# Kernel optimization log

Hardware: AMD Instinct MI355X
Metric: run time of the kernel (lower is better)

Reference implementation:

```python
import jax, jax.numpy as jnp
import numpy as np

NEG_SLOPE = 0.2   # PyG GATConv default negative_slope
LN_EPS = 1e-5
SOFTMAX_EPS = 1e-16  # PyG softmax denominator eps


def setup_inputs() -> dict:
    key = jax.random.key(0)
    ks = jax.random.split(key, 6)
    N, IN, OUT, H, E = 100000, 128, 64, 2, 1600000
    X = jax.random.normal(ks[0], (N, IN), dtype=jnp.float32)
    edge_index = jax.random.randint(ks[1], (2, E), 0, N, dtype=jnp.int64)
    W = jax.random.normal(ks[2], (H * OUT, IN), dtype=jnp.float32) * 0.05
    att_src = jax.random.normal(ks[3], (H, OUT), dtype=jnp.float32) * 0.05
    att_dst = jax.random.normal(ks[4], (H, OUT), dtype=jnp.float32) * 0.05
    bias = jnp.zeros((OUT,), dtype=jnp.float32)
    ln_gamma = jnp.ones((OUT,), dtype=jnp.float32)
    ln_beta = jnp.zeros((OUT,), dtype=jnp.float32)
    return {"X": X, "edge_index": edge_index, "W": W, "att_src": att_src,
            "att_dst": att_dst, "bias": bias, "ln_gamma": ln_gamma, "ln_beta": ln_beta}


def reference(X, edge_index, W, att_src, att_dst, bias, ln_gamma, ln_beta):
    N = X.shape[0]
    H, F = att_src.shape
    # PyG GATConv default: add self-loops
    loops = jnp.arange(N, dtype=edge_index.dtype)
    src = jnp.concatenate([edge_index[0], loops])  # [Et]
    dst = jnp.concatenate([edge_index[1], loops])  # [Et]
    # linear projection: x' = X @ W^T  -> [N, H, F]
    x = (X @ W.T).reshape(N, H, F)
    # per-node attention logits  [N, H]
    a_src = jnp.einsum('nhf,hf->nh', x, att_src)
    a_dst = jnp.einsum('nhf,hf->nh', x, att_dst)
    # per-edge logits, leaky relu  [Et, H]
    e = jax.nn.leaky_relu(a_src[src] + a_dst[dst], NEG_SLOPE)
    # segment softmax over incoming edges of each dst node
    m = jax.ops.segment_max(e, dst, num_segments=N)          # [N, H]
    ex = jnp.exp(e - m[dst])
    denom = jax.ops.segment_sum(ex, dst, num_segments=N)     # [N, H]
    alpha = ex / (denom[dst] + SOFTMAX_EPS)                  # [Et, H]
    # weighted scatter-add of source features
    msg = x[src] * alpha[:, :, None]                         # [Et, H, F]
    out = jax.ops.segment_sum(msg, dst, num_segments=N)      # [N, H, F]
    # concat=False -> mean over heads, then bias
    out = out.mean(axis=1) + bias                            # [N, F]
    # LayerNorm over features
    mu = out.mean(axis=-1, keepdims=True)
    var = ((out - mu) ** 2).mean(axis=-1, keepdims=True)
    h = (out - mu) * jax.lax.rsqrt(var + LN_EPS) * ln_gamma + ln_beta
    return h
```

## Files before the change

kernel.cpp:

```cpp
#include <hip/hip_runtime.h>
#include <hip/hip_bf16.h>

#define NEG_SLOPE 0.2f
#define LN_EPS 1e-5f
#define SM_EPS 1e-16f

typedef __attribute__((ext_vector_type(8))) short bf16x8;
typedef __attribute__((ext_vector_type(4))) float f32x4;

__device__ inline unsigned short f2bf(float f) {
    unsigned u = __float_as_uint(f);
    return (unsigned short)((u + 0x7FFFu + ((u >> 16) & 1u)) >> 16);
}
__device__ inline float bf_lo(unsigned int v) { return __uint_as_float(v << 16); }
__device__ inline float bf_hi(unsigned int v) { return __uint_as_float(v & 0xffff0000u); }

#define NBIN 512
#define SORT_CHUNK 4096

__global__ __launch_bounds__(256) void k_gemm(const float* __restrict__ X,
                                              const float* __restrict__ W,
                                              const float* __restrict__ att_src,
                                              const float* __restrict__ att_dst,
                                              unsigned int* __restrict__ xp,
                                              float2* __restrict__ aS,
                                              float2* __restrict__ aD, int N) {
    __shared__ unsigned short Ws[128 * 136];
    __shared__ unsigned short Xs[64 * 136];
    const int t = threadIdx.x;
    const int b0 = blockIdx.x * 64;
    const int lane = t & 63;
    const int w = t >> 6;
    const int c15 = lane & 15;
    const int quad = lane >> 4;

#pragma unroll
    for (int i = 0; i < 16; ++i) {
        int f = i * 256 + t;
        int nr = f >> 5;
        int q = f & 31;
        float4 v = reinterpret_cast<const float4*>(W)[nr * 32 + q];
        ushort4 b;
        b.x = f2bf(v.x); b.y = f2bf(v.y); b.z = f2bf(v.z); b.w = f2bf(v.w);
        *reinterpret_cast<ushort4*>(&Ws[nr * 136 + q * 4]) = b;
    }
#pragma unroll
    for (int i = 0; i < 8; ++i) {
        int f = i * 256 + t;
        int m = f >> 5;
        int q = f & 31;
        int gr = b0 + m;
        if (gr >= N) gr = N - 1;
        float4 v = reinterpret_cast<const float4*>(X)[(size_t)gr * 32 + q];
        ushort4 b;
        b.x = f2bf(v.x); b.y = f2bf(v.y); b.z = f2bf(v.z); b.w = f2bf(v.w);
        *reinterpret_cast<ushort4*>(&Xs[m * 136 + q * 4]) = b;
    }
    __syncthreads();

    f32x4 acc[8];
#pragma unroll
    for (int ct = 0; ct < 8; ++ct) acc[ct] = (f32x4){0.f, 0.f, 0.f, 0.f};

#pragma unroll
    for (int kc = 0; kc < 4; ++kc) {
        bf16x8 af = *reinterpret_cast<const bf16x8*>(
            &Xs[(w * 16 + c15) * 136 + kc * 32 + quad * 8]);
#pragma unroll
        for (int ct = 0; ct < 8; ++ct) {
            bf16x8 bfr = *reinterpret_cast<const bf16x8*>(
                &Ws[(ct * 16 + c15) * 136 + kc * 32 + quad * 8]);
            acc[ct] = __builtin_amdgcn_mfma_f32_16x16x32_bf16(af, bfr, acc[ct], 0, 0, 0);
        }
    }

    float attS[8], attD[8];
#pragma unroll
    for (int ct = 0; ct < 8; ++ct) {
        attS[ct] = att_src[ct * 16 + c15];
        attD[ct] = att_dst[ct * 16 + c15];
    }

#pragma unroll
    for (int r = 0; r < 4; ++r) {
        int row = b0 + w * 16 + quad * 4 + r;
        float s0 = 0.f, s1 = 0.f, d0 = 0.f, d1 = 0.f;
#pragma unroll
        for (int ct = 0; ct < 4; ++ct) {
            s0 += acc[ct][r] * attS[ct];
            d0 += acc[ct][r] * attD[ct];
            s1 += acc[ct + 4][r] * attS[ct + 4];
            d1 += acc[ct + 4][r] * attD[ct + 4];
        }
#pragma unroll
        for (int o = 1; o < 16; o <<= 1) {
            s0 += __shfl_xor(s0, o);
            s1 += __shfl_xor(s1, o);
            d0 += __shfl_xor(d0, o);
            d1 += __shfl_xor(d1, o);
        }
        if (row < N) {
#pragma unroll
            for (int ct = 0; ct < 4; ++ct) {
                unsigned int p = (unsigned int)f2bf(acc[ct][r]) |
                                 ((unsigned int)f2bf(acc[ct + 4][r]) << 16);
                xp[(size_t)row * 64 + ct * 16 + c15] = p;
            }
            if (c15 == 0) {
                aS[row] = make_float2(s0, s1);
                aD[row] = make_float2(d0, d1);
            }
        }
    }
}

__global__ __launch_bounds__(256) void k_uw(const int* __restrict__ ei,
                                            const float2* __restrict__ aS,
                                            const float2* __restrict__ aD,
                                            unsigned int* __restrict__ uW,
                                            int* __restrict__ binTotal, int E) {
    __shared__ int hist[NBIN];
    const int t = threadIdx.x;
    for (int i = t; i < NBIN; i += 256) hist[i] = 0;
    __syncthreads();
    const int base = blockIdx.x * 2048;
#pragma unroll
    for (int k = 0; k < 8; ++k) {
        int i = base + k * 256 + t;
        if (i < E) {
            int s = ei[i];
            int d = ei[E + i];
            float2 a = aS[s];
            float2 ad2 = aD[d];
            float f0 = a.x + ad2.x; f0 = fmaxf(f0, NEG_SLOPE * f0);
            float f1 = a.y + ad2.y; f1 = fmaxf(f1, NEG_SLOPE * f1);
            uW[i] = (unsigned int)f2bf(__expf(f0)) |
                    ((unsigned int)f2bf(__expf(f1)) << 16);
            atomicAdd(&hist[d >> 8], 1);
        }
    }
    __syncthreads();
    for (int i = t; i < NBIN; i += 256)
        if (hist[i]) atomicAdd(&binTotal[i], hist[i]);
}

__global__ __launch_bounds__(512) void k_binscan(const int* __restrict__ binTotal,
                                                 int* __restrict__ binStart,
                                                 int* __restrict__ binCursor, int E) {
    __shared__ int buf[NBIN];
    const int t = threadIdx.x;
    int v = binTotal[t];
    buf[t] = v;
    __syncthreads();
    for (int o = 1; o < NBIN; o <<= 1) {
        int u = (t >= o) ? buf[t - o] : 0;
        __syncthreads();
        buf[t] += u;
        __syncthreads();
    }
    int excl = buf[t] - v;
    binStart[t] = excl;
    binCursor[t] = excl;
    if (t == NBIN - 1) binStart[NBIN] = buf[t];
}

__global__ __launch_bounds__(256) void k_scatter(const int* __restrict__ ei,
                                                 const unsigned int* __restrict__ uW,
                                                 int* __restrict__ binCursor,
                                                 uint2* __restrict__ tmp, int E) {
    __shared__ int off[NBIN];
    const int t = threadIdx.x;
    const int base = blockIdx.x * SORT_CHUNK;

    int se[16], de[16];
    unsigned int ue[16];
#pragma unroll
    for (int k = 0; k < 16; ++k) {
        int i = base + k * 256 + t;
        if (i < E) {
            se[k] = ei[i];
            de[k] = ei[E + i];
            ue[k] = uW[i];
        } else {
            de[k] = -1;
        }
    }

    for (int i = t; i < NBIN; i += 256) off[i] = 0;
    __syncthreads();
#pragma unroll
    for (int k = 0; k < 16; ++k)
        if (de[k] >= 0) atomicAdd(&off[de[k] >> 8], 1);
    __syncthreads();
    for (int i = t; i < NBIN; i += 256) {
        int h = off[i];
        off[i] = h ? atomicAdd(&binCursor[i], h) : 0;
    }
    __syncthreads();
#pragma unroll
    for (int k = 0; k < 16; ++k) {
        if (de[k] >= 0) {
            int p = atomicAdd(&off[de[k] >> 8], 1);
            tmp[p] = make_uint2(((unsigned)(de[k] & 255) << 24) | (unsigned)se[k],
                                ue[k]);
        }
    }
}

__global__ __launch_bounds__(256) void k_bucket(const uint2* __restrict__ tmp,
                                                const int* __restrict__ binStart,
                                                const float2* __restrict__ aS,
                                                const float2* __restrict__ aD,
                                                uint2* __restrict__ csr,
                                                int* __restrict__ row_ptr,
                                                float2* __restrict__ metaN,
                                                int E, int N) {
    __shared__ int cnt[256];
    __shared__ int cur[256];
    __shared__ int lds[4];
    const int t = threadIdx.x;
    const int b = blockIdx.x;
    const int start = binStart[b];
    const int end = binStart[b + 1];
    const int m = end - start;

    cnt[t] = 0;
    __syncthreads();
    for (int k = t; k < m; k += 256) {
        uint2 e = tmp[start + k];
        atomicAdd(&cnt[e.x >> 24], 1);
    }
    __syncthreads();

    int v = cnt[t];
    int lane = t & 63, w = t >> 6;
    int incl = v;
#pragma unroll
    for (int o = 1; o < 64; o <<= 1) {
        int u = __shfl_up(incl, o);
        if (lane >= o) incl += u;
    }
    if (lane == 63) lds[w] = incl;
    __syncthreads();
    if (t == 0) {
        int run = 0;
        for (int i = 0; i < 4; ++i) { int tv = lds[i]; lds[i] = run; run += tv; }
    }
    __syncthreads();
    int excl = lds[w] + incl - v;
    cur[t] = start + excl;

    int d = b * 256 + t;
    if (d < N) {
        float2 a = aS[d];
        float2 ad2 = aD[d];
        float f0 = a.x + ad2.x; f0 = fmaxf(f0, NEG_SLOPE * f0);
        float f1 = a.y + ad2.y; f1 = fmaxf(f1, NEG_SLOPE * f1);
        metaN[d] = make_float2(__expf(f0), __expf(f1));
        row_ptr[d] = start + excl;
    }
    if (b == 0 && t == 0) row_ptr[N] = E;
    __syncthreads();

    for (int k = t; k < m; k += 256) {
        uint2 e = tmp[start + k];
        int p = atomicAdd(&cur[e.x >> 24], 1);
        csr[p] = make_uint2(e.x & 0x00FFFFFFu, e.y);
    }
}

__global__ __launch_bounds__(256) void k_agg(const unsigned int* __restrict__ xp,
                                             const float2* __restrict__ metaN,
                                             const int* __restrict__ row_ptr,
                                             const uint2* __restrict__ csr,
                                             const float* __restrict__ bias,
                                             const float* __restrict__ gamma,
                                             const float* __restrict__ beta,
                                             float* __restrict__ out, int N) {
    const int w = threadIdx.x >> 6, lane = threadIdx.x & 63;
    const int n = blockIdx.x * 4 + w;
    if (n >= N) return;

    float2 meta = metaN[n];
    unsigned int vself = xp[(size_t)n * 64 + lane];
    float S0 = meta.x * bf_lo(vself);
    float S1 = meta.y * bf_hi(vself);
    float D0 = meta.x, D1 = meta.y;

    const int jb = row_ptr[n], je = row_ptr[n + 1];
    int j = jb;
    for (; j + 7 < je; j += 8) {
        int ju = __builtin_amdgcn_readfirstlane(j);
        uint2 c[8];
#pragma unroll
        for (int q = 0; q < 8; ++q) c[q] = csr[ju + q];
        unsigned int v[8];
#pragma unroll
        for (int q = 0; q < 8; ++q) v[q] = xp[(size_t)c[q].x * 64 + lane];
#pragma unroll
        for (int q = 0; q < 8; ++q) {
            float u0 = bf_lo(c[q].y), u1 = bf_hi(c[q].y);
            S0 += u0 * bf_lo(v[q]);
            S1 += u1 * bf_hi(v[q]);
            D0 += u0; D1 += u1;
        }
    }
    for (; j + 3 < je; j += 4) {
        int ju = __builtin_amdgcn_readfirstlane(j);
        uint2 c[4];
#pragma unroll
        for (int q = 0; q < 4; ++q) c[q] = csr[ju + q];
        unsigned int v[4];
#pragma unroll
        for (int q = 0; q < 4; ++q) v[q] = xp[(size_t)c[q].x * 64 + lane];
#pragma unroll
        for (int q = 0; q < 4; ++q) {
            float u0 = bf_lo(c[q].y), u1 = bf_hi(c[q].y);
            S0 += u0 * bf_lo(v[q]);
            S1 += u1 * bf_hi(v[q]);
            D0 += u0; D1 += u1;
        }
    }
    for (; j < je; ++j) {
        uint2 c = csr[__builtin_amdgcn_readfirstlane(j)];
        unsigned int vv = xp[(size_t)c.x * 64 + lane];
        float u0 = bf_lo(c.y), u1 = bf_hi(c.y);
        S0 += u0 * bf_lo(vv);
        S1 += u1 * bf_hi(vv);
        D0 += u0; D1 += u1;
    }

    float inv0 = 0.5f / (D0 + SM_EPS);
    float inv1 = 0.5f / (D1 + SM_EPS);
    float o = inv0 * S0 + inv1 * S1 + bias[lane];

    float mu = o;
#pragma unroll
    for (int d = 32; d > 0; d >>= 1) mu += __shfl_xor(mu, d);
    mu *= (1.0f / 64.0f);
    float dv = o - mu;
    float var = dv * dv;
#pragma unroll
    for (int d = 32; d > 0; d >>= 1) var += __shfl_xor(var, d);
    var *= (1.0f / 64.0f);
    out[(size_t)n * 64 + lane] = dv * rsqrtf(var + LN_EPS) * gamma[lane] + beta[lane];
}

extern "C" void kernel_launch(void* const* d_in, const int* in_sizes, int n_in,
                              void* d_out, int out_size, void* d_ws, size_t ws_size,
                              hipStream_t stream) {
    const float* X        = (const float*)d_in[0];
    const int*   ei       = (const int*)d_in[1];
    const float* W        = (const float*)d_in[2];
    const float* att_src  = (const float*)d_in[3];
    const float* att_dst  = (const float*)d_in[4];
    const float* bias     = (const float*)d_in[5];
    const float* ln_gamma = (const float*)d_in[6];
    const float* ln_beta  = (const float*)d_in[7];
    float* out = (float*)d_out;

    const int N = in_sizes[0] / 128;
    const int E = in_sizes[1] / 2;
    const int NBUCK = (N + 255) / 256;

    char* ws = (char*)d_ws;
    size_t off = 0;
    auto alloc = [&](size_t bytes) {
        size_t o = off;
        off += (bytes + 255) & ~(size_t)255;
        return o;
    };
    unsigned int* xp     = (unsigned int*)(ws + alloc((size_t)N * 64 * 4));
    float2* aS           = (float2*)(ws + alloc((size_t)N * 8));
    float2* aD           = (float2*)(ws + alloc((size_t)N * 8));
    float2* metaN        = (float2*)(ws + alloc((size_t)N * 8));
    int* row_ptr         = (int*)(ws + alloc((size_t)(N + 1) * 4));
    uint2* csr           = (uint2*)(ws + alloc((size_t)E * 8));
    uint2* tmp           = (uint2*)(ws + alloc((size_t)E * 8));
    unsigned int* uW     = (unsigned int*)(ws + alloc((size_t)E * 4));
    int* binTotal        = (int*)(ws + alloc((NBIN + 1) * 4));
    int* binStart        = (int*)(ws + alloc((NBIN + 1) * 4));
    int* binCursor       = (int*)(ws + alloc(NBIN * 4));

    hipMemsetAsync(binTotal, 0, NBIN * 4, stream);

    k_gemm<<<(N + 63) / 64, 256, 0, stream>>>(X, W, att_src, att_dst, xp, aS, aD, N);
    k_uw<<<(E + 2047) / 2048, 256, 0, stream>>>(ei, aS, aD, uW, binTotal, E);
    k_binscan<<<1, 512, 0, stream>>>(binTotal, binStart, binCursor, E);
    k_scatter<<<(E + SORT_CHUNK - 1) / SORT_CHUNK, 256, 0, stream>>>(ei, uW, binCursor, tmp, E);
    k_bucket<<<NBUCK, 256, 0, stream>>>(tmp, binStart, aS, aD, csr, row_ptr,
                                        metaN, E, N);
    k_agg<<<(N + 3) / 4, 256, 0, stream>>>(xp, metaN, row_ptr, csr,
                                           bias, ln_gamma, ln_beta, out, N);
}
```

Before: 252.1 us.

## Fuse edge weighting into scatter with fixed-capacity bins and precompute denominators

```diff
diff --git a/kernel.cpp b/kernel.cpp
--- a/kernel.cpp
+++ b/kernel.cpp
@@ -15,8 +15,9 @@
 __device__ inline float bf_lo(unsigned int v) { return __uint_as_float(v << 16); }
 __device__ inline float bf_hi(unsigned int v) { return __uint_as_float(v & 0xffff0000u); }
 
-#define NBIN 512
-#define SORT_CHUNK 4096
+#define NBIN 1024
+#define BCAP 2560
+#define SCHUNK 2048
 
 __global__ __launch_bounds__(256) void k_gemm(const float* __restrict__ X,
                                               const float* __restrict__ W,
@@ -24,7 +25,8 @@
                                               const float* __restrict__ att_dst,
                                               unsigned int* __restrict__ xp,
                                               float2* __restrict__ aS,
-                                              float2* __restrict__ aD, int N) {
+                                              float2* __restrict__ aD,
+                                              int* __restrict__ binCursor, int N) {
     __shared__ unsigned short Ws[128 * 136];
     __shared__ unsigned short Xs[64 * 136];
     const int t = threadIdx.x;
@@ -33,6 +35,10 @@
     const int w = t >> 6;
     const int c15 = lane & 15;
     const int quad = lane >> 4;
+
+    if (blockIdx.x == 0) {
+        for (int i = t; i < NBIN; i += 256) binCursor[i] = i * BCAP;
+    }
 
 #pragma unroll
     for (int i = 0; i < 16; ++i) {
@@ -114,73 +120,30 @@
     }
 }
 
-__global__ __launch_bounds__(256) void k_uw(const int* __restrict__ ei,
-                                            const float2* __restrict__ aS,
-                                            const float2* __restrict__ aD,
-                                            unsigned int* __restrict__ uW,
-                                            int* __restrict__ binTotal, int E) {
-    __shared__ int hist[NBIN];
+__global__ __launch_bounds__(256) void k_scatter(const int* __restrict__ ei,
+                                                 const float2* __restrict__ aS,
+                                                 const float2* __restrict__ aD,
+                                                 int* __restrict__ binCursor,
+                                                 uint2* __restrict__ tmp, int E) {
+    __shared__ int off[NBIN];
     const int t = threadIdx.x;
-    for (int i = t; i < NBIN; i += 256) hist[i] = 0;
-    __syncthreads();
-    const int base = blockIdx.x * 2048;
+    const int base = blockIdx.x * SCHUNK;
+
+    int se[8], de[8];
+    unsigned int ue[8];
 #pragma unroll
     for (int k = 0; k < 8; ++k) {
         int i = base + k * 256 + t;
         if (i < E) {
             int s = ei[i];
             int d = ei[E + i];
+            se[k] = s; de[k] = d;
             float2 a = aS[s];
             float2 ad2 = aD[d];
             float f0 = a.x + ad2.x; f0 = fmaxf(f0, NEG_SLOPE * f0);
             float f1 = a.y + ad2.y; f1 = fmaxf(f1, NEG_SLOPE * f1);
-            uW[i] = (unsigned int)f2bf(__expf(f0)) |
+            ue[k] = (unsigned int)f2bf(__expf(f0)) |
                     ((unsigned int)f2bf(__expf(f1)) << 16);
-            atomicAdd(&hist[d >> 8], 1);
-        }
-    }
-    __syncthreads();
-    for (int i = t; i < NBIN; i += 256)
-        if (hist[i]) atomicAdd(&binTotal[i], hist[i]);
-}
-
-__global__ __launch_bounds__(512) void k_binscan(const int* __restrict__ binTotal,
-                                                 int* __restrict__ binStart,
-                                                 int* __restrict__ binCursor, int E) {
-    __shared__ int buf[NBIN];
-    const int t = threadIdx.x;
-    int v = binTotal[t];
-    buf[t] = v;
-    __syncthreads();
-    for (int o = 1; o < NBIN; o <<= 1) {
-        int u = (t >= o) ? buf[t - o] : 0;
-        __syncthreads();
-        buf[t] += u;
-        __syncthreads();
-    }
-    int excl = buf[t] - v;
-    binStart[t] = excl;
-    binCursor[t] = excl;
-    if (t == NBIN - 1) binStart[NBIN] = buf[t];
-}
-
-__global__ __launch_bounds__(256) void k_scatter(const int* __restrict__ ei,
-                                                 const unsigned int* __restrict__ uW,
-                                                 int* __restrict__ binCursor,
-                                                 uint2* __restrict__ tmp, int E) {
-    __shared__ int off[NBIN];
-    const int t = threadIdx.x;
-    const int base = blockIdx.x * SORT_CHUNK;
-
-    int se[16], de[16];
-    unsigned int ue[16];
-#pragma unroll
-    for (int k = 0; k < 16; ++k) {
-        int i = base + k * 256 + t;
-        if (i < E) {
-            se[k] = ei[i];
-            de[k] = ei[E + i];
-            ue[k] = uW[i];
         } else {
             de[k] = -1;
         }
@@ -189,8 +152,8 @@
     for (int i = t; i < NBIN; i += 256) off[i] = 0;
     __syncthreads();
 #pragma unroll
-    for (int k = 0; k < 16; ++k)
-        if (de[k] >= 0) atomicAdd(&off[de[k] >> 8], 1);
+    for (int k = 0; k < 8; ++k)
+        if (de[k] >= 0) atomicAdd(&off[de[k] >> 7], 1);
     __syncthreads();
     for (int i = t; i < NBIN; i += 256) {
         int h = off[i];
@@ -198,80 +161,90 @@
     }
     __syncthreads();
 #pragma unroll
-    for (int k = 0; k < 16; ++k) {
+    for (int k = 0; k < 8; ++k) {
         if (de[k] >= 0) {
-            int p = atomicAdd(&off[de[k] >> 8], 1);
-            tmp[p] = make_uint2(((unsigned)(de[k] & 255) << 24) | (unsigned)se[k],
+            int p = atomicAdd(&off[de[k] >> 7], 1);
+            tmp[p] = make_uint2(((unsigned)(de[k] & 127) << 24) | (unsigned)se[k],
                                 ue[k]);
         }
     }
 }
 
 __global__ __launch_bounds__(256) void k_bucket(const uint2* __restrict__ tmp,
-                                                const int* __restrict__ binStart,
+                                                const int* __restrict__ binCursor,
                                                 const float2* __restrict__ aS,
                                                 const float2* __restrict__ aD,
                                                 uint2* __restrict__ csr,
-                                                int* __restrict__ row_ptr,
-                                                float2* __restrict__ metaN,
-                                                int E, int N) {
-    __shared__ int cnt[256];
-    __shared__ int cur[256];
-    __shared__ int lds[4];
+                                                unsigned int* __restrict__ rowPtr,
+                                                float4* __restrict__ metaN, int N) {
+    __shared__ uint2 ebuf[BCAP];
+    __shared__ int cnt[128];
+    __shared__ int cur[128];
+    __shared__ float den0[128], den1[128];
+    __shared__ int lds2[2];
     const int t = threadIdx.x;
     const int b = blockIdx.x;
-    const int start = binStart[b];
-    const int end = binStart[b + 1];
-    const int m = end - start;
-
-    cnt[t] = 0;
-    __syncthreads();
+    const int start = b * BCAP;
+    int m = binCursor[b] - start;
+    if (m > BCAP) m = BCAP;
+
+    if (t < 128) { cnt[t] = 0; den0[t] = 0.f; den1[t] = 0.f; }
+    __syncthreads();
+
     for (int k = t; k < m; k += 256) {
         uint2 e = tmp[start + k];
-        atomicAdd(&cnt[e.x >> 24], 1);
-    }
-    __syncthreads();
-
-    int v = cnt[t];
-    int lane = t & 63, w = t >> 6;
-    int incl = v;
-#pragma unroll
-    for (int o = 1; o < 64; o <<= 1) {
-        int u = __shfl_up(incl, o);
-        if (lane >= o) incl += u;
-    }
-    if (lane == 63) lds[w] = incl;
-    __syncthreads();
-    if (t == 0) {
-        int run = 0;
-        for (int i = 0; i < 4; ++i) { int tv = lds[i]; lds[i] = run; run += tv; }
-    }
-    __syncthreads();
-    int excl = lds[w] + incl - v;
-    cur[t] = start + excl;
-
-    int d = b * 256 + t;
-    if (d < N) {
-        float2 a = aS[d];
-        float2 ad2 = aD[d];
-        float f0 = a.x + ad2.x; f0 = fmaxf(f0, NEG_SLOPE * f0);
-        float f1 = a.y + ad2.y; f1 = fmaxf(f1, NEG_SLOPE * f1);
-        metaN[d] = make_float2(__expf(f0), __expf(f1));
-        row_ptr[d] = start + excl;
-    }
-    if (b == 0 && t == 0) row_ptr[N] = E;
+        ebuf[k] = e;
+        int li = e.x >> 24;
+        atomicAdd(&cnt[li], 1);
+        atomicAdd(&den0[li], bf_lo(e.y));
+        atomicAdd(&den1[li], bf_hi(e.y));
+    }
+    __syncthreads();
+
+    int v = 0, incl = 0;
+    const int lane = t & 63, w = t >> 6;
+    if (t < 128) {
+        v = cnt[t];
+        incl = v;
+#pragma unroll
+        for (int o = 1; o < 64; o <<= 1) {
+            int u = __shfl_up(incl, o);
+            if (lane >= o) incl += u;
+        }
+        if (lane == 63) lds2[w] = incl;
+    }
+    __syncthreads();
+    if (t == 0) { int a = lds2[0]; lds2[0] = 0; lds2[1] = a; }
+    __syncthreads();
+    if (t < 128) {
+        int excl = lds2[w] + incl - v;
+        cur[t] = excl;
+        int d = b * 128 + t;
+        if (d < N) {
+            float2 a = aS[d];
+            float2 ad2 = aD[d];
+            float f0 = a.x + ad2.x; f0 = fmaxf(f0, NEG_SLOPE * f0);
+            float f1 = a.y + ad2.y; f1 = fmaxf(f1, NEG_SLOPE * f1);
+            float ws0 = __expf(f0), ws1 = __expf(f1);
+            float D0 = den0[t] + ws0, D1 = den1[t] + ws1;
+            metaN[d] = make_float4(ws0, ws1,
+                                   0.5f / (D0 + SM_EPS), 0.5f / (D1 + SM_EPS));
+            rowPtr[d] = (unsigned)(start + excl) | ((unsigned)v << 22);
+        }
+    }
     __syncthreads();
 
     for (int k = t; k < m; k += 256) {
-        uint2 e = tmp[start + k];
-        int p = atomicAdd(&cur[e.x >> 24], 1);
-        csr[p] = make_uint2(e.x & 0x00FFFFFFu, e.y);
+        uint2 e = ebuf[k];
+        int li = e.x >> 24;
+        int p = atomicAdd(&cur[li], 1);
+        csr[start + p] = make_uint2(e.x & 0x00FFFFFFu, e.y);
     }
 }
 
 __global__ __launch_bounds__(256) void k_agg(const unsigned int* __restrict__ xp,
-                                             const float2* __restrict__ metaN,
-                                             const int* __restrict__ row_ptr,
+                                             const float4* __restrict__ metaN,
+                                             const unsigned int* __restrict__ rowPtr,
                                              const uint2* __restrict__ csr,
                                              const float* __restrict__ bias,
                                              const float* __restrict__ gamma,
@@ -281,13 +254,14 @@
     const int n = blockIdx.x * 4 + w;
     if (n >= N) return;
 
-    float2 meta = metaN[n];
+    float4 meta = metaN[n];
     unsigned int vself = xp[(size_t)n * 64 + lane];
     float S0 = meta.x * bf_lo(vself);
     float S1 = meta.y * bf_hi(vself);
-    float D0 = meta.x, D1 = meta.y;
-
-    const int jb = row_ptr[n], je = row_ptr[n + 1];
+
+    unsigned int pr = rowPtr[n];
+    const int jb = (int)(pr & 0x3FFFFFu);
+    const int je = jb + (int)(pr >> 22);
     int j = jb;
     for (; j + 7 < je; j += 8) {
         int ju = __builtin_amdgcn_readfirstlane(j);
@@ -299,10 +273,8 @@
         for (int q = 0; q < 8; ++q) v[q] = xp[(size_t)c[q].x * 64 + lane];
 #pragma unroll
         for (int q = 0; q < 8; ++q) {
-            float u0 = bf_lo(c[q].y), u1 = bf_hi(c[q].y);
-            S0 += u0 * bf_lo(v[q]);
-            S1 += u1 * bf_hi(v[q]);
-            D0 += u0; D1 += u1;
+            S0 += bf_lo(c[q].y) * bf_lo(v[q]);
+            S1 += bf_hi(c[q].y) * bf_hi(v[q]);
         }
     }
     for (; j + 3 < je; j += 4) {
@@ -315,24 +287,18 @@
         for (int q = 0; q < 4; ++q) v[q] = xp[(size_t)c[q].x * 64 + lane];
 #pragma unroll
         for (int q = 0; q < 4; ++q) {
-            float u0 = bf_lo(c[q].y), u1 = bf_hi(c[q].y);
-            S0 += u0 * bf_lo(v[q]);
-            S1 += u1 * bf_hi(v[q]);
-            D0 += u0; D1 += u1;
+            S0 += bf_lo(c[q].y) * bf_lo(v[q]);
+            S1 += bf_hi(c[q].y) * bf_hi(v[q]);
         }
     }
     for (; j < je; ++j) {
         uint2 c = csr[__builtin_amdgcn_readfirstlane(j)];
         unsigned int vv = xp[(size_t)c.x * 64 + lane];
-        float u0 = bf_lo(c.y), u1 = bf_hi(c.y);
-        S0 += u0 * bf_lo(vv);
-        S1 += u1 * bf_hi(vv);
-        D0 += u0; D1 += u1;
-    }
-
-    float inv0 = 0.5f / (D0 + SM_EPS);
-    float inv1 = 0.5f / (D1 + SM_EPS);
-    float o = inv0 * S0 + inv1 * S1 + bias[lane];
+        S0 += bf_lo(c.y) * bf_lo(vv);
+        S1 += bf_hi(c.y) * bf_hi(vv);
+    }
+
+    float o = meta.z * S0 + meta.w * S1 + bias[lane];
 
     float mu = o;
 #pragma unroll
@@ -361,7 +327,7 @@
 
     const int N = in_sizes[0] / 128;
     const int E = in_sizes[1] / 2;
-    const int NBUCK = (N + 255) / 256;
+    const int NBUCK = (N + 127) / 128;
 
     char* ws = (char*)d_ws;
     size_t off = 0;
@@ -373,23 +339,18 @@
     unsigned int* xp     = (unsigned int*)(ws + alloc((size_t)N * 64 * 4));
     float2* aS           = (float2*)(ws + alloc((size_t)N * 8));
     float2* aD           = (float2*)(ws + alloc((size_t)N * 8));
-    float2* metaN        = (float2*)(ws + alloc((size_t)N * 8));
-    int* row_ptr         = (int*)(ws + alloc((size_t)(N + 1) * 4));
-    uint2* csr           = (uint2*)(ws + alloc((size_t)E * 8));
-    uint2* tmp           = (uint2*)(ws + alloc((size_t)E * 8));
-    unsigned int* uW     = (unsigned int*)(ws + alloc((size_t)E * 4));
-    int* binTotal        = (int*)(ws + alloc((NBIN + 1) * 4));
-    int* binStart        = (int*)(ws + alloc((NBIN + 1) * 4));
+    float4* metaN        = (float4*)(ws + alloc((size_t)N * 16));
+    unsigned int* rowPtr = (unsigned int*)(ws + alloc((size_t)N * 4));
+    uint2* csr           = (uint2*)(ws + alloc((size_t)NBIN * BCAP * 8));
+    uint2* tmp           = (uint2*)(ws + alloc((size_t)NBIN * BCAP * 8));
     int* binCursor       = (int*)(ws + alloc(NBIN * 4));
 
-    hipMemsetAsync(binTotal, 0, NBIN * 4, stream);
-
-    k_gemm<<<(N + 63) / 64, 256, 0, stream>>>(X, W, att_src, att_dst, xp, aS, aD, N);
-    k_uw<<<(E + 2047) / 2048, 256, 0, stream>>>(ei, aS, aD, uW, binTotal, E);
-    k_binscan<<<1, 512, 0, stream>>>(binTotal, binStart, binCursor, E);
-    k_scatter<<<(E + SORT_CHUNK - 1) / SORT_CHUNK, 256, 0, stream>>>(ei, uW, binCursor, tmp, E);
-    k_bucket<<<NBUCK, 256, 0, stream>>>(tmp, binStart, aS, aD, csr, row_ptr,
-                                        metaN, E, N);
-    k_agg<<<(N + 3) / 4, 256, 0, stream>>>(xp, metaN, row_ptr, csr,
+    k_gemm<<<(N + 63) / 64, 256, 0, stream>>>(X, W, att_src, att_dst, xp, aS, aD,
+                                              binCursor, N);
+    k_scatter<<<(E + SCHUNK - 1) / SCHUNK, 256, 0, stream>>>(ei, aS, aD,
+                                                             binCursor, tmp, E);
+    k_bucket<<<NBUCK, 256, 0, stream>>>(tmp, binCursor, aS, aD, csr, rowPtr,
+                                        metaN, N);
+    k_agg<<<(N + 3) / 4, 256, 0, stream>>>(xp, metaN, rowPtr, csr,
                                            bias, ln_gamma, ln_beta, out, N);
 }
```

Measured after the change: 252.6 us. No clear change (+0.2%).
